# Kernel tuning notes

Measured on AMD Instinct MI355X. Metric: run time of the kernel, lower is better.

## Reference

```python
import jax, jax.numpy as jnp
import numpy as np

B = 1000        # graphs in batch
T_PER = 250     # tasks per graph
M_PER = 50      # machines per graph
N_T = B * T_PER
N_M = B * M_PER
D_T = 16        # INPUT_TASK_DIM
D_M = 8         # INPUT_MACHINE_DIM
H = 128         # hidden_dim
IN_PREV_IDX = 0
TASK_FEAT_IDX = 1
EPS = 1e-5      # BatchNorm eps


def _mk_params(rng):
    def lin(i, o):
        return (rng.standard_normal((i, o)).astype(np.float32) / np.sqrt(i),
                np.zeros(o, np.float32))
    p = {}
    p['bn_t_gamma'] = np.ones(D_T, np.float32); p['bn_t_beta'] = np.zeros(D_T, np.float32)
    p['Wt1'], p['bt1'] = lin(D_T, H); p['Wt2'], p['bt2'] = lin(H, H)
    p['bn_m_gamma'] = np.ones(D_M, np.float32); p['bn_m_beta'] = np.zeros(D_M, np.float32)
    p['Wm1'], p['bm1'] = lin(D_M, H); p['Wm2'], p['bm2'] = lin(H, H)
    p['Wa1'], p['ba1'] = lin(2 * H, H); p['Wa2'], p['ba2'] = lin(H, H)
    p['Wl1'], p['bl1'] = lin(3 * H, H); p['Wl2'], p['bl2'] = lin(H, H)
    p['Wo1'], p['bo1'] = lin(H, H); p['Wo2'], p['bo2'] = lin(H, 1)
    return p


def setup_inputs() -> dict:
    rng = np.random.default_rng(0)
    xt = rng.standard_normal((N_T, D_T)).astype(np.float32)
    # prev-task flag: even task ids are 'prev'
    xt[:, IN_PREV_IDX] = (np.arange(N_T) % 2 == 0).astype(np.float32)
    # per-graph machine assignment in [0, M_PER), or -1 (unassigned) every 10th task
    lm = rng.integers(0, M_PER, N_T)
    lm[np.arange(N_T) % 10 == 0] = -1
    xt[:, TASK_FEAT_IDX] = lm.astype(np.float32)
    xm = rng.standard_normal((N_M, D_M)).astype(np.float32)
    inp = {'x_tasks': jnp.asarray(xt), 'x_machines': jnp.asarray(xm)}
    inp.update({k: jnp.asarray(v) for k, v in _mk_params(rng).items()})
    inp['x_tasks_batch'] = jnp.asarray(np.repeat(np.arange(B), T_PER).astype(np.int32))
    inp['x_machines_batch'] = jnp.asarray(np.repeat(np.arange(B), M_PER).astype(np.int32))
    # labels are tasks 0,5,10,...; prev tasks are even ids -> prev-local index t//2
    # label tasks that are prev: t % 10 == 0 -> prev_tasks_label_idx = 5*arange(N_T//10)
    inp['label_idx'] = jnp.asarray((5 * np.arange(N_T // 10)).astype(np.int32))
    inp['num_graphs'] = B
    return inp


def _bn(x, g, b):
    # BatchNorm1d in training mode: biased batch stats
    mu = x.mean(axis=0)
    var = x.var(axis=0)
    return g * (x - mu) * jax.lax.rsqrt(var + EPS) + b


def _seg_mean(x, seg, n):
    s = jax.ops.segment_sum(x, seg, num_segments=n)
    c = jax.ops.segment_sum(jnp.ones((x.shape[0], 1), x.dtype), seg, num_segments=n)
    return s / jnp.maximum(c, 1.0)


def reference(x_tasks, x_machines, bn_t_gamma, bn_t_beta, Wt1, bt1, Wt2, bt2,
              bn_m_gamma, bn_m_beta, Wm1, bm1, Wm2, bm2,
              Wa1, ba1, Wa2, ba2, Wl1, bl1, Wl2, bl2,
              Wo1, bo1, Wo2, bo2,
              x_tasks_batch, x_machines_batch, label_idx, num_graphs):
    nm = x_machines.shape[0]
    # tasks_select_assignment: local machine id -> global machine row (or pad row nm)
    tm_col = x_tasks[:, TASK_FEAT_IDX]
    cnt_m = jnp.bincount(x_machines_batch, length=num_graphs)
    cum = jnp.cumsum(cnt_m) - cnt_m  # cumulative machines per graph
    task_m = jnp.where(tm_col == -1.0, nm,
                       tm_col.astype(jnp.int32) + cum[x_tasks_batch].astype(jnp.int32))
    # node embeddings: BN -> Linear -> ReLU -> Linear -> ReLU
    th = jax.nn.relu(jax.nn.relu(_bn(x_tasks, bn_t_gamma, bn_t_beta) @ Wt1 + bt1) @ Wt2 + bt2)
    mh = jax.nn.relu(jax.nn.relu(_bn(x_machines, bn_m_gamma, bn_m_beta) @ Wm1 + bm1) @ Wm2 + bm2)
    # global aggregation per graph (scatter_mean) + MLP
    aggr = jnp.concatenate([_seg_mean(th, x_tasks_batch, num_graphs),
                            _seg_mean(mh, x_machines_batch, num_graphs)], axis=1)
    aggr = jax.nn.relu(aggr @ Wa1 + ba1) @ Wa2 + ba2
    # gather machine embedding per task (pad row of zeros for unassigned)
    mh_pad = jnp.concatenate([mh, jnp.zeros((1, H), mh.dtype)], axis=0)
    cat = jnp.concatenate([th, aggr[x_tasks_batch], mh_pad[task_m]], axis=1)  # [N_T, 3H]
    h = jax.nn.relu(cat @ Wl1 + bl1) @ Wl2 + bl2
    out = (jax.nn.relu(h @ Wo1 + bo1) @ Wo2 + bo2)[label_idx]
    return out
```

## Files before the change

### kernel.cpp

```cpp
#include <hip/hip_runtime.h>
#include <hip/hip_bf16.h>

constexpr int B     = 1000;
constexpr int T_PER = 250;
constexpr int M_PER = 50;
constexpr int N_T   = B * T_PER;
constexpr int N_M   = B * M_PER;
constexpr int H     = 128;
constexpr int N_LBL = 25000;
constexpr float EPS = 1e-05f;

constexpr int NB_T = 256;
constexpr int NB_M = 64;
constexpr int NB_P = 64;

constexpr int OFF_PART_T = 0;
constexpr int OFF_PART_M = OFF_PART_T + NB_T * 32;
constexpr int OFF_AT     = OFF_PART_M + NB_M * 16;
constexpr int OFF_BT     = OFF_AT + 16;
constexpr int OFF_AM     = OFF_BT + 16;
constexpr int OFF_BM     = OFF_AM + 8;
constexpr int OFF_BT1F   = OFF_BM + 8;
constexpr int OFF_BM1F   = OFF_BT1F + 128;
constexpr int OFF_MEANT  = OFF_BM1F + 128;
constexpr int OFF_MEANM  = OFF_MEANT + B * H;
constexpr int OFF_HALF   = OFF_MEANM + B * H;
constexpr int HO_WT1  = 0;
constexpr int HO_WT2  = 4096;
constexpr int HO_WM1  = 20480;
constexpr int HO_WM2  = 24576;
constexpr int HO_WA1  = 40960;
constexpr int HO_WA2  = 73728;
constexpr int HO_WL1  = 90112;
constexpr int HO_WL2  = 139264;
constexpr int HO_WO1  = 155648;

typedef _Float16 f16x8 __attribute__((ext_vector_type(8)));
typedef _Float16 f16x4 __attribute__((ext_vector_type(4)));
typedef float f32x4 __attribute__((ext_vector_type(4)));

#define MFMA16(a, b, c) __builtin_amdgcn_mfma_f32_16x16x32_f16(a, b, c, 0, 0, 0)

template <int C, int NB>
__device__ __forceinline__ void stats_body(const float* __restrict__ x, int nelem,
                                           float* __restrict__ part, int blk, int t,
                                           float* ls, float* lq) {
    float s = 0.f, q = 0.f;
    for (int e = blk * 256 + t; e < nelem; e += NB * 256) {
        float v = x[e];
        s += v;
        q += v * v;
    }
    ls[t] = s; lq[t] = q;
    __syncthreads();
    if (t < C) {
        float S = 0.f, Q = 0.f;
        for (int u = t; u < 256; u += C) { S += ls[u]; Q += lq[u]; }
        part[blk * 2 * C + t] = S;
        part[blk * 2 * C + C + t] = Q;
    }
}

__device__ __forceinline__ void cvt_tr(const float* __restrict__ src, _Float16* __restrict__ dst,
                                       int K, int Kp, int tid, int nt) {
    for (int idx = tid; idx < 128 * Kp; idx += nt) {
        int c = idx / Kp, k = idx - c * Kp;
        float v = (k < K) ? src[k * 128 + c] : 0.f;
        dst[idx] = (_Float16)v;
    }
}

__global__ __launch_bounds__(256) void stats_prep_kernel(
        const float* __restrict__ xt, const float* __restrict__ xm,
        const float* __restrict__ Wt1, const float* __restrict__ Wt2,
        const float* __restrict__ Wm1, const float* __restrict__ Wm2,
        const float* __restrict__ Wa1, const float* __restrict__ Wa2,
        const float* __restrict__ Wl1, const float* __restrict__ Wl2,
        const float* __restrict__ Wo1,
        float* __restrict__ wsf, _Float16* __restrict__ wh) {
    __shared__ float ls[256], lq[256];
    const int bid = blockIdx.x, t = threadIdx.x;
    if (bid < NB_T) {
        stats_body<16, NB_T>(xt, N_T * 16, wsf + OFF_PART_T, bid, t, ls, lq);
    } else if (bid < NB_T + NB_M) {
        stats_body<8, NB_M>(xm, N_M * 8, wsf + OFF_PART_M, bid - NB_T, t, ls, lq);
    } else {
        const int tid = (bid - NB_T - NB_M) * 256 + t;
        const int nt = NB_P * 256;
        cvt_tr(Wt1, wh + HO_WT1, 16, 32, tid, nt);
        cvt_tr(Wt2, wh + HO_WT2, 128, 128, tid, nt);
        cvt_tr(Wm1, wh + HO_WM1, 8, 32, tid, nt);
        cvt_tr(Wm2, wh + HO_WM2, 128, 128, tid, nt);
        cvt_tr(Wa1, wh + HO_WA1, 256, 256, tid, nt);
        cvt_tr(Wa2, wh + HO_WA2, 128, 128, tid, nt);
        cvt_tr(Wl1, wh + HO_WL1, 384, 384, tid, nt);
        cvt_tr(Wl2, wh + HO_WL2, 128, 128, tid, nt);
        cvt_tr(Wo1, wh + HO_WO1, 128, 128, tid, nt);
    }
}

__global__ __launch_bounds__(256) void finalize_kernel(
        const float* __restrict__ gt, const float* __restrict__ btb,
        const float* __restrict__ gm, const float* __restrict__ bmb,
        const float* __restrict__ Wt1, const float* __restrict__ bt1,
        const float* __restrict__ Wm1, const float* __restrict__ bm1,
        float* __restrict__ ws) {
    __shared__ float red[256];
    __shared__ float statT[32], statM[16];
    __shared__ float shT[16], shM[8];
    const int t = threadIdx.x;
    {
        const int slot = t & 31, chunk = t >> 5;
        const float* p = ws + OFF_PART_T;
        float s = 0.f;
        for (int b = chunk * 32; b < chunk * 32 + 32; b++) s += p[b * 32 + slot];
        red[t] = s;
    }
    __syncthreads();
    if (t < 32) {
        float v = 0.f;
#pragma unroll
        for (int c = 0; c < 8; c++) v += red[t + 32 * c];
        statT[t] = v;
    }
    __syncthreads();
    {
        float s = 0.f;
        if (t < 128) {
            const int slot = t & 15, chunk = t >> 4;
            const float* p = ws + OFF_PART_M;
            for (int b = chunk * 8; b < chunk * 8 + 8; b++) s += p[b * 16 + slot];
        }
        red[t] = s;
    }
    __syncthreads();
    if (t < 16) {
        float v = 0.f;
#pragma unroll
        for (int c = 0; c < 8; c++) v += red[t + 16 * c];
        statM[t] = v;
    }
    __syncthreads();
    if (t < 16) {
        float mu  = statT[t] / (float)N_T;
        float var = statT[16 + t] / (float)N_T - mu * mu;
        float a   = gt[t] * rsqrtf(var + EPS);
        ws[OFF_AT + t] = a;
        float b = btb[t] - mu * a;
        ws[OFF_BT + t] = b;
        shT[t] = b;
    } else if (t < 24) {
        int c = t - 16;
        float mu  = statM[c] / (float)N_M;
        float var = statM[8 + c] / (float)N_M - mu * mu;
        float a   = gm[c] * rsqrtf(var + EPS);
        ws[OFF_AM + c] = a;
        float b = bmb[c] - mu * a;
        ws[OFF_BM + c] = b;
        shM[c] = b;
    }
    __syncthreads();
    if (t < 128) {
        float s = bt1[t];
#pragma unroll
        for (int k = 0; k < 16; k++) s += shT[k] * Wt1[k * 128 + t];
        ws[OFF_BT1F + t] = s;
    } else {
        int c = t - 128;
        float s = bm1[c];
#pragma unroll
        for (int k = 0; k < 8; k++) s += shM[k] * Wm1[k * 128 + c];
        ws[OFF_BM1F + c] = s;
    }
}

__device__ __forceinline__ void zacc(f32x4 acc[4][2]) {
#pragma unroll
    for (int rg = 0; rg < 4; rg++)
#pragma unroll
        for (int mi = 0; mi < 2; mi++) acc[rg][mi] = (f32x4){0.f, 0.f, 0.f, 0.f};
}

__device__ __forceinline__ void ld32(f16x8 w[2], const _Float16* __restrict__ WT,
                                     int m0, int r, int gq) {
#pragma unroll
    for (int mi = 0; mi < 2; mi++)
        w[mi] = *(const f16x8*)(WT + ((m0 + mi) * 16 + r) * 32 + gq * 8);
}

__device__ __forceinline__ void ld128(f16x8 w[2][4], const _Float16* __restrict__ WT,
                                      int lda, int k0, int m0, int r, int gq) {
#pragma unroll
    for (int mi = 0; mi < 2; mi++)
#pragma unroll
        for (int ks = 0; ks < 4; ks++)
            w[mi][ks] = *(const f16x8*)(WT + ((m0 + mi) * 16 + r) * lda + k0 + ks * 32 + gq * 8);
}

__device__ __forceinline__ void mm32(const f16x8 w[2], const _Float16* __restrict__ act,
                                     int rstride, int r, int gq, f32x4 acc[4][2]) {
#pragma unroll
    for (int rg = 0; rg < 4; rg++) {
        const f16x8 bf = *(const f16x8*)(act + (rg * 16 + r) * rstride + gq * 8);
        acc[rg][0] = MFMA16(w[0], bf, acc[rg][0]);
        acc[rg][1] = MFMA16(w[1], bf, acc[rg][1]);
    }
}

__device__ __forceinline__ void mm128(const f16x8 w[2][4], const _Float16* __restrict__ act,
                                      int rstride, int r, int gq, f32x4 acc[4][2]) {
#pragma unroll
    for (int rg = 0; rg < 4; rg++)
#pragma unroll
        for (int ks = 0; ks < 4; ks++) {
            const f16x8 bf = *(const f16x8*)(act + (rg * 16 + r) * rstride + ks * 32 + gq * 8);
            acc[rg][0] = MFMA16(w[0][ks], bf, acc[rg][0]);
            acc[rg][1] = MFMA16(w[1][ks], bf, acc[rg][1]);
        }
}

__device__ __forceinline__ void epi_cs(const f32x4 acc[4][2], const f32x4 bv[2],
                                       _Float16* __restrict__ dst, int dstride,
                                       int m0, int r, int gq, bool relu) {
#pragma unroll
    for (int rg = 0; rg < 4; rg++)
#pragma unroll
        for (int mi = 0; mi < 2; mi++) {
            f16x4 hv;
#pragma unroll
            for (int j = 0; j < 4; j++) {
                float v = acc[rg][mi][j] + bv[mi][j];
                if (relu) v = fmaxf(v, 0.f);
                hv[j] = (_Float16)v;
            }
            *(f16x4*)(dst + (rg * 16 + r) * dstride + (m0 + mi) * 16 + gq * 4) = hv;
        }
}

template <int CIN, int ROWS, int PASSES>
__device__ __forceinline__ void seg_body(const float* __restrict__ x, const float* __restrict__ scaleA,
        const _Float16* __restrict__ W1T, const float* __restrict__ b1,
        const _Float16* __restrict__ W2T, const float* __restrict__ b2,
        float* __restrict__ meanout, int g, int t,
        _Float16* __restrict__ xs, _Float16* __restrict__ h1s) {
    const int lane = t & 63, wave = t >> 6;
    const int r = lane & 15, gq = lane >> 4;
    const int m0 = 2 * wave;
    f16x8 w1[2], w2[2][4];
    ld32(w1, W1T, m0, r, gq);
    ld128(w2, W2T, 128, 0, m0, r, gq);
    f32x4 b1v[2], b2v[2];
#pragma unroll
    for (int mi = 0; mi < 2; mi++) {
        b1v[mi] = *(const f32x4*)(b1 + (m0 + mi) * 16 + gq * 4);
        b2v[mi] = *(const f32x4*)(b2 + (m0 + mi) * 16 + gq * 4);
    }
    const int jrow = (CIN == 16) ? (t >> 2) : (t >> 1);
    const int part = (CIN == 16) ? (t & 3) : (t & 1);
    const bool stager = (CIN == 16) ? true : (t < 128);
    f32x4 av = {0.f, 0.f, 0.f, 0.f};
    if (stager) av = *(const f32x4*)(scaleA + part * 4);
    f16x4 z4; z4[0] = z4[1] = z4[2] = z4[3] = (_Float16)0.f;
    if (stager) {
        if (CIN == 16) {
            *(f16x4*)(xs + jrow * 40 + 16 + part * 4) = z4;
        } else {
#pragma unroll
            for (int q = 0; q < 3; q++)
                *(f16x4*)(xs + jrow * 40 + 8 + part * 12 + q * 4) = z4;
        }
    }
    float4 xr = {0.f, 0.f, 0.f, 0.f};
    if (stager) {
        int cl = (jrow < ROWS) ? jrow : (ROWS - 1);
        xr = *(const float4*)(x + (g * ROWS + cl) * CIN + part * 4);
    }
    f32x4 rs[2];
    rs[0] = (f32x4){0.f, 0.f, 0.f, 0.f};
    rs[1] = (f32x4){0.f, 0.f, 0.f, 0.f};
    for (int p = 0; p < PASSES; p++) {
        if (stager) {
            const bool valid = (p * 64 + jrow) < ROWS;
            f16x4 hv;
            hv[0] = (_Float16)(valid ? av[0] * xr.x : 0.f);
            hv[1] = (_Float16)(valid ? av[1] * xr.y : 0.f);
            hv[2] = (_Float16)(valid ? av[2] * xr.z : 0.f);
            hv[3] = (_Float16)(valid ? av[3] * xr.w : 0.f);
            *(f16x4*)(xs + jrow * 40 + part * 4) = hv;
        }
        __syncthreads();
        if (p + 1 < PASSES && stager) {
            int lr = (p + 1) * 64 + jrow;
            int cl = (lr < ROWS) ? lr : (ROWS - 1);
            xr = *(const float4*)(x + (g * ROWS + cl) * CIN + part * 4);
        }
        f32x4 acc[4][2];
        zacc(acc);
        mm32(w1, xs, 40, r, gq, acc);
        epi_cs(acc, b1v, h1s, 136, m0, r, gq, true);
        __syncthreads();
        zacc(acc);
        mm128(w2, h1s, 136, r, gq, acc);
#pragma unroll
        for (int rg = 0; rg < 4; rg++) {
            const bool vr = (p * 64 + rg * 16 + r) < ROWS;
#pragma unroll
            for (int mi = 0; mi < 2; mi++)
#pragma unroll
                for (int j = 0; j < 4; j++) {
                    float v = fmaxf(acc[rg][mi][j] + b2v[mi][j], 0.f);
                    rs[mi][j] += vr ? v : 0.f;
                }
        }
    }
#pragma unroll
    for (int mi = 0; mi < 2; mi++)
#pragma unroll
        for (int j = 0; j < 4; j++) {
            float v = rs[mi][j];
            v += __shfl_xor(v, 1); v += __shfl_xor(v, 2);
            v += __shfl_xor(v, 4); v += __shfl_xor(v, 8);
            rs[mi][j] = v;
        }
    if (r == 0) {
        constexpr float inv = 1.f / (float)ROWS;
#pragma unroll
        for (int mi = 0; mi < 2; mi++) {
            f32x4 st = rs[mi] * inv;
            *(f32x4*)(meanout + g * H + (m0 + mi) * 16 + gq * 4) = st;
        }
    }
}

__global__ __launch_bounds__(256) void seg_fused(const float* __restrict__ xt, const float* __restrict__ xm,
        const _Float16* __restrict__ wh, const float* __restrict__ wsf,
        const float* __restrict__ bt2, const float* __restrict__ bm2,
        float* __restrict__ meanT, float* __restrict__ meanM) {
    __shared__ __attribute__((aligned(16))) _Float16 xs[64 * 40];
    __shared__ __attribute__((aligned(16))) _Float16 h1s[64 * 136];
    if (blockIdx.x < B)
        seg_body<16, T_PER, 4>(xt, wsf + OFF_AT, wh + HO_WT1, wsf + OFF_BT1F,
                               wh + HO_WT2, bt2, meanT, blockIdx.x, threadIdx.x, xs, h1s);
    else
        seg_body<8, M_PER, 1>(xm, wsf + OFF_AM, wh + HO_WM1, wsf + OFF_BM1F,
                              wh + HO_WM2, bm2, meanM, blockIdx.x - B, threadIdx.x, xs, h1s);
}

__global__ __launch_bounds__(256) void aggr_kernel(const float* __restrict__ meanT, const float* __restrict__ meanM,
        const _Float16* __restrict__ Wa1T, const float* __restrict__ ba1,
        const _Float16* __restrict__ Wa2T, const float* __restrict__ ba2,
        const _Float16* __restrict__ Wl1T, const float* __restrict__ bl1,
        float* __restrict__ agg2) {
    __shared__ __attribute__((aligned(16))) _Float16 cin[16 * 264];
    __shared__ __attribute__((aligned(16))) _Float16 h1s[16 * 136];
    __shared__ __attribute__((aligned(16))) _Float16 ags[16 * 136];
    const int t = threadIdx.x, lane = t & 63, wave = t >> 6;
    const int r = lane & 15, gq = lane >> 4;
    const int m0 = 2 * wave;
    const int g0 = blockIdx.x * 16;
    f16x8 wa1[2][8], wa2[2][4], wl1b[2][4];
#pragma unroll
    for (int mi = 0; mi < 2; mi++)
#pragma unroll
        for (int ks = 0; ks < 8; ks++)
            wa1[mi][ks] = *(const f16x8*)(Wa1T + ((m0 + mi) * 16 + r) * 256 + ks * 32 + gq * 8);
    ld128(wa2, Wa2T, 128, 0, m0, r, gq);
    ld128(wl1b, Wl1T, 384, 128, m0, r, gq);
    f32x4 b1v[2], b2v[2], blv[2];
#pragma unroll
    for (int mi = 0; mi < 2; mi++) {
        b1v[mi] = *(const f32x4*)(ba1 + (m0 + mi) * 16 + gq * 4);
        b2v[mi] = *(const f32x4*)(ba2 + (m0 + mi) * 16 + gq * 4);
        blv[mi] = *(const f32x4*)(bl1 + (m0 + mi) * 16 + gq * 4);
    }
    for (int e = t; e < 16 * 64; e += 256) {
        int j = e >> 6, c4 = e & 63;
        int g = g0 + j;
        float4 v = {0.f, 0.f, 0.f, 0.f};
        if (g < B) v = (c4 < 32) ? *(const float4*)(meanT + g * H + c4 * 4)
                                 : *(const float4*)(meanM + g * H + (c4 - 32) * 4);
        f16x4 hv;
        hv[0] = (_Float16)v.x; hv[1] = (_Float16)v.y; hv[2] = (_Float16)v.z; hv[3] = (_Float16)v.w;
        *(f16x4*)(cin + j * 264 + c4 * 4) = hv;
    }
    __syncthreads();
    f32x4 a0 = {0.f, 0.f, 0.f, 0.f}, a1 = {0.f, 0.f, 0.f, 0.f};
    {
        const _Float16* bp = cin + r * 264 + gq * 8;
#pragma unroll
        for (int ks = 0; ks < 8; ks++) {
            const f16x8 bf = *(const f16x8*)(bp + ks * 32);
            a0 = MFMA16(wa1[0][ks], bf, a0);
            a1 = MFMA16(wa1[1][ks], bf, a1);
        }
    }
    {
        f16x4 h0, h1v;
#pragma unroll
        for (int j = 0; j < 4; j++) {
            h0[j]  = (_Float16)fmaxf(a0[j] + b1v[0][j], 0.f);
            h1v[j] = (_Float16)fmaxf(a1[j] + b1v[1][j], 0.f);
        }
        *(f16x4*)(h1s + r * 136 + m0 * 16 + gq * 4) = h0;
        *(f16x4*)(h1s + r * 136 + (m0 + 1) * 16 + gq * 4) = h1v;
    }
    __syncthreads();
    a0 = (f32x4){0.f, 0.f, 0.f, 0.f}; a1 = (f32x4){0.f, 0.f, 0.f, 0.f};
    {
        const _Float16* bp = h1s + r * 136 + gq * 8;
#pragma unroll
        for (int ks = 0; ks < 4; ks++) {
            const f16x8 bf = *(const f16x8*)(bp + ks * 32);
            a0 = MFMA16(wa2[0][ks], bf, a0);
            a1 = MFMA16(wa2[1][ks], bf, a1);
        }
    }
    {
        f16x4 h0, h1v;
#pragma unroll
        for (int j = 0; j < 4; j++) {
            h0[j]  = (_Float16)(a0[j] + b2v[0][j]);
            h1v[j] = (_Float16)(a1[j] + b2v[1][j]);
        }
        *(f16x4*)(ags + r * 136 + m0 * 16 + gq * 4) = h0;
        *(f16x4*)(ags + r * 136 + (m0 + 1) * 16 + gq * 4) = h1v;
    }
    __syncthreads();
    a0 = (f32x4){0.f, 0.f, 0.f, 0.f}; a1 = (f32x4){0.f, 0.f, 0.f, 0.f};
    {
        const _Float16* bp = ags + r * 136 + gq * 8;
#pragma unroll
        for (int ks = 0; ks < 4; ks++) {
            const f16x8 bf = *(const f16x8*)(bp + ks * 32);
            a0 = MFMA16(wl1b[0][ks], bf, a0);
            a1 = MFMA16(wl1b[1][ks], bf, a1);
        }
    }
    if (g0 + r < B) {
        *(f32x4*)(agg2 + (g0 + r) * H + m0 * 16 + gq * 4) = a0 + blv[0];
        *(f32x4*)(agg2 + (g0 + r) * H + (m0 + 1) * 16 + gq * 4) = a1 + blv[1];
    }
}

__global__ __launch_bounds__(256) void label_kernel(
        const float* __restrict__ xt, const float* __restrict__ xm,
        const float* __restrict__ scT, const float* __restrict__ scM,
        const _Float16* __restrict__ Wt1T, const float* __restrict__ bt1f,
        const _Float16* __restrict__ Wt2T, const float* __restrict__ bt2,
        const _Float16* __restrict__ Wm1T, const float* __restrict__ bm1f,
        const _Float16* __restrict__ Wm2T, const float* __restrict__ bm2,
        const _Float16* __restrict__ Wl1T,
        const _Float16* __restrict__ Wl2T, const float* __restrict__ bl2,
        const _Float16* __restrict__ Wo1T, const float* __restrict__ bo1,
        const float* __restrict__ Wo2, const float* __restrict__ bo2,
        const float* __restrict__ agg2,
        const int* __restrict__ tbatch, const int* __restrict__ lidx,
        float* __restrict__ out) {
    __shared__ __attribute__((aligned(16))) _Float16 xs_t[64 * 40];
    __shared__ __attribute__((aligned(16))) _Float16 xs_m[64 * 40];
    __shared__ __attribute__((aligned(16))) _Float16 h1s[64 * 136];
    __shared__ __attribute__((aligned(16))) _Float16 cat[64 * 264];
    __shared__ float psum[4][64];
    __shared__ int ridx[64], gidx[64], midx[64];
    const int t = threadIdx.x;
    const int lane = t & 63, wave = t >> 6;
    const int r = lane & 15, gq = lane >> 4;
    const int m0 = 2 * wave;
    if (t < 64) {
        int i = blockIdx.x * 64 + t;
        int rr = (i < N_LBL) ? lidx[i] : 0;
        ridx[t] = rr;
        int gg = tbatch[rr];
        gidx[t] = gg;
        float tv = xt[rr * 16 + 1];
        midx[t] = (tv == -1.0f) ? -1 : ((int)tv + gg * M_PER);
    }
    __syncthreads();
    f16x4 z4; z4[0] = z4[1] = z4[2] = z4[3] = (_Float16)0.f;
    {
        int j = t >> 2, part = t & 3;
        f32x4 avt = *(const f32x4*)(scT + part * 4);
        float4 v = *(const float4*)(xt + ridx[j] * 16 + part * 4);
        f16x4 hv;
        hv[0] = (_Float16)(avt[0] * v.x); hv[1] = (_Float16)(avt[1] * v.y);
        hv[2] = (_Float16)(avt[2] * v.z); hv[3] = (_Float16)(avt[3] * v.w);
        *(f16x4*)(xs_t + j * 40 + part * 4) = hv;
        *(f16x4*)(xs_t + j * 40 + 16 + part * 4) = z4;
    }
    if (t < 128) {
        int j = t >> 1, part = t & 1;
        f32x4 avm = *(const f32x4*)(scM + part * 4);
        int m = midx[j];
        f16x4 hv = z4;
        if (m >= 0) {
            float4 v = *(const float4*)(xm + m * 8 + part * 4);
            hv[0] = (_Float16)(avm[0] * v.x); hv[1] = (_Float16)(avm[1] * v.y);
            hv[2] = (_Float16)(avm[2] * v.z); hv[3] = (_Float16)(avm[3] * v.w);
        }
        *(f16x4*)(xs_m + j * 40 + part * 4) = hv;
#pragma unroll
        for (int q = 0; q < 3; q++)
            *(f16x4*)(xs_m + j * 40 + 8 + part * 12 + q * 4) = z4;
    }
    __syncthreads();
    f32x4 agg2v[4][2];
#pragma unroll
    for (int rg = 0; rg < 4; rg++)
#pragma unroll
        for (int mi = 0; mi < 2; mi++)
            agg2v[rg][mi] = *(const f32x4*)(agg2 + gidx[rg * 16 + r] * H + (m0 + mi) * 16 + gq * 4);
    f32x4 acc[4][2];
    f16x8 wt1[2]; ld32(wt1, Wt1T, m0, r, gq);
    f16x8 wt2[2][4]; ld128(wt2, Wt2T, 128, 0, m0, r, gq);
    f32x4 bva[2], bvb[2];
#pragma unroll
    for (int mi = 0; mi < 2; mi++) {
        bva[mi] = *(const f32x4*)(bt1f + (m0 + mi) * 16 + gq * 4);
        bvb[mi] = *(const f32x4*)(bt2 + (m0 + mi) * 16 + gq * 4);
    }
    zacc(acc);
    mm32(wt1, xs_t, 40, r, gq, acc);
    epi_cs(acc, bva, h1s, 136, m0, r, gq, true);
    f16x8 wm1[2]; ld32(wm1, Wm1T, m0, r, gq);
    __syncthreads();
    zacc(acc);
    mm128(wt2, h1s, 136, r, gq, acc);
    epi_cs(acc, bvb, cat, 264, m0, r, gq, true);
    f16x8 wm2[2][4]; ld128(wm2, Wm2T, 128, 0, m0, r, gq);
    __syncthreads();
#pragma unroll
    for (int mi = 0; mi < 2; mi++) {
        bva[mi] = *(const f32x4*)(bm1f + (m0 + mi) * 16 + gq * 4);
        bvb[mi] = *(const f32x4*)(bm2 + (m0 + mi) * 16 + gq * 4);
    }
    zacc(acc);
    mm32(wm1, xs_m, 40, r, gq, acc);
    epi_cs(acc, bva, h1s, 136, m0, r, gq, true);
    f16x8 wl1a[2][4]; ld128(wl1a, Wl1T, 384, 0, m0, r, gq);
    __syncthreads();
    zacc(acc);
    mm128(wm2, h1s, 136, r, gq, acc);
#pragma unroll
    for (int rg = 0; rg < 4; rg++) {
        const bool sent = (midx[rg * 16 + r] < 0);
#pragma unroll
        for (int mi = 0; mi < 2; mi++) {
            f16x4 hv;
#pragma unroll
            for (int j = 0; j < 4; j++) {
                float v = fmaxf(acc[rg][mi][j] + bvb[mi][j], 0.f);
                hv[j] = (_Float16)(sent ? 0.f : v);
            }
            *(f16x4*)(cat + (rg * 16 + r) * 264 + 128 + (m0 + mi) * 16 + gq * 4) = hv;
        }
    }
    f16x8 wl1c[2][4]; ld128(wl1c, Wl1T, 384, 256, m0, r, gq);
    __syncthreads();
    zacc(acc);
    mm128(wl1a, cat, 264, r, gq, acc);
    mm128(wl1c, cat + 128, 264, r, gq, acc);
#pragma unroll
    for (int rg = 0; rg < 4; rg++)
#pragma unroll
        for (int mi = 0; mi < 2; mi++) {
            f16x4 hv;
#pragma unroll
            for (int j = 0; j < 4; j++)
                hv[j] = (_Float16)fmaxf(acc[rg][mi][j] + agg2v[rg][mi][j], 0.f);
            *(f16x4*)(h1s + (rg * 16 + r) * 136 + (m0 + mi) * 16 + gq * 4) = hv;
        }
    f16x8 wl2[2][4]; ld128(wl2, Wl2T, 128, 0, m0, r, gq);
    __syncthreads();
#pragma unroll
    for (int mi = 0; mi < 2; mi++) bva[mi] = *(const f32x4*)(bl2 + (m0 + mi) * 16 + gq * 4);
    zacc(acc);
    mm128(wl2, h1s, 136, r, gq, acc);
    epi_cs(acc, bva, cat, 264, m0, r, gq, false);
    f16x8 wo1[2][4]; ld128(wo1, Wo1T, 128, 0, m0, r, gq);
    __syncthreads();
#pragma unroll
    for (int mi = 0; mi < 2; mi++) bva[mi] = *(const f32x4*)(bo1 + (m0 + mi) * 16 + gq * 4);
    f32x4 wo2v[2];
#pragma unroll
    for (int mi = 0; mi < 2; mi++) wo2v[mi] = *(const f32x4*)(Wo2 + (m0 + mi) * 16 + gq * 4);
    zacc(acc);
    mm128(wo1, cat, 264, r, gq, acc);
#pragma unroll
    for (int rg = 0; rg < 4; rg++) {
        float pv = 0.f;
#pragma unroll
        for (int mi = 0; mi < 2; mi++)
#pragma unroll
            for (int j = 0; j < 4; j++)
                pv += fmaxf(acc[rg][mi][j] + bva[mi][j], 0.f) * wo2v[mi][j];
        pv += __shfl_xor(pv, 16);
        pv += __shfl_xor(pv, 32);
        if (lane < 16) psum[wave][rg * 16 + lane] = pv;
    }
    __syncthreads();
    if (t < 64) {
        int i = blockIdx.x * 64 + t;
        if (i < N_LBL)
            out[i] = psum[0][t] + psum[1][t] + psum[2][t] + psum[3][t] + bo2[0];
    }
}

extern "C" void kernel_launch(void* const* d_in, const int* in_sizes, int n_in,
                              void* d_out, int out_size, void* d_ws, size_t ws_size,
                              hipStream_t stream) {
    const float* xt  = (const float*)d_in[0];
    const float* xm  = (const float*)d_in[1];
    const float* gt  = (const float*)d_in[2];
    const float* btb = (const float*)d_in[3];
    const float* Wt1 = (const float*)d_in[4];  const float* bt1 = (const float*)d_in[5];
    const float* Wt2 = (const float*)d_in[6];  const float* bt2 = (const float*)d_in[7];
    const float* gm  = (const float*)d_in[8];  const float* bmb = (const float*)d_in[9];
    const float* Wm1 = (const float*)d_in[10]; const float* bm1 = (const float*)d_in[11];
    const float* Wm2 = (const float*)d_in[12]; const float* bm2 = (const float*)d_in[13];
    const float* Wa1 = (const float*)d_in[14]; const float* ba1 = (const float*)d_in[15];
    const float* Wa2 = (const float*)d_in[16]; const float* ba2 = (const float*)d_in[17];
    const float* Wl1 = (const float*)d_in[18]; const float* bl1 = (const float*)d_in[19];
    const float* Wl2 = (const float*)d_in[20]; const float* bl2 = (const float*)d_in[21];
    const float* Wo1 = (const float*)d_in[22]; const float* bo1 = (const float*)d_in[23];
    const float* Wo2 = (const float*)d_in[24]; const float* bo2 = (const float*)d_in[25];
    const int* tb  = (const int*)d_in[26];
    const int* lix = (const int*)d_in[28];
    float* wsf = (float*)d_ws;
    _Float16* wh = (_Float16*)(wsf + OFF_HALF);
    float* outp = (float*)d_out;

    stats_prep_kernel<<<NB_T + NB_M + NB_P, 256, 0, stream>>>(
        xt, xm, Wt1, Wt2, Wm1, Wm2, Wa1, Wa2, Wl1, Wl2, Wo1, wsf, wh);
    finalize_kernel<<<1, 256, 0, stream>>>(gt, btb, gm, bmb, Wt1, bt1, Wm1, bm1, wsf);
    seg_fused<<<2 * B, 256, 0, stream>>>(xt, xm, wh, wsf, bt2, bm2,
                                         wsf + OFF_MEANT, wsf + OFF_MEANM);
    aggr_kernel<<<(B + 15) / 16, 256, 0, stream>>>(wsf + OFF_MEANT, wsf + OFF_MEANM,
                                                   wh + HO_WA1, ba1, wh + HO_WA2, ba2,
                                                   wh + HO_WL1, bl1, wsf + OFF_MEANT);
    label_kernel<<<(N_LBL + 63) / 64, 256, 0, stream>>>(xt, xm,
                                                        wsf + OFF_AT, wsf + OFF_AM,
                                                        wh + HO_WT1, wsf + OFF_BT1F, wh + HO_WT2, bt2,
                                                        wh + HO_WM1, wsf + OFF_BM1F, wh + HO_WM2, bm2,
                                                        wh + HO_WL1,
                                                        wh + HO_WL2, bl2,
                                                        wh + HO_WO1, bo1, Wo2, bo2,
                                                        wsf + OFF_MEANT, tb, lix, outp);
}
```

Baseline: 74.12 us.

## Rewrite segment-mean MLP as per-wave register-resident MFMA pipeline with pre-converted fp16 inputs

```diff
diff --git a/kernel.cpp b/kernel.cpp
--- a/kernel.cpp
+++ b/kernel.cpp
@@ -1,5 +1,4 @@
 #include <hip/hip_runtime.h>
-#include <hip/hip_bf16.h>
 
 constexpr int B     = 1000;
 constexpr int T_PER = 250;
@@ -34,15 +33,19 @@
 constexpr int HO_WL1  = 90112;
 constexpr int HO_WL2  = 139264;
 constexpr int HO_WO1  = 155648;
+constexpr int HO_XT16 = 172032;
+constexpr int HO_XM16 = HO_XT16 + N_T * 16;
 
 typedef _Float16 f16x8 __attribute__((ext_vector_type(8)));
 typedef _Float16 f16x4 __attribute__((ext_vector_type(4)));
 typedef float f32x4 __attribute__((ext_vector_type(4)));
 
-#define MFMA16(a, b, c) __builtin_amdgcn_mfma_f32_16x16x32_f16(a, b, c, 0, 0, 0)
+#define MFMA16(a, b, c)   __builtin_amdgcn_mfma_f32_16x16x32_f16(a, b, c, 0, 0, 0)
+#define MFMAK16(a, b, c)  __builtin_amdgcn_mfma_f32_16x16x16f16(a, b, c, 0, 0, 0)
 
 template <int C, int NB>
-__device__ __forceinline__ void stats_body(const float* __restrict__ x, int nelem,
+__device__ __forceinline__ void stats_body(const float* __restrict__ x,
+                                           _Float16* __restrict__ x16, int nelem,
                                            float* __restrict__ part, int blk, int t,
                                            float* ls, float* lq) {
     float s = 0.f, q = 0.f;
@@ -50,6 +53,7 @@
         float v = x[e];
         s += v;
         q += v * v;
+        x16[e] = (_Float16)v;
     }
     ls[t] = s; lq[t] = q;
     __syncthreads();
@@ -72,8 +76,8 @@
 
 __global__ __launch_bounds__(256) void stats_prep_kernel(
         const float* __restrict__ xt, const float* __restrict__ xm,
-        const float* __restrict__ Wt1, const float* __restrict__ Wt2,
-        const float* __restrict__ Wm1, const float* __restrict__ Wm2,
+        _Float16* __restrict__ xt16, _Float16* __restrict__ xm16,
+        const float* __restrict__ Wt2, const float* __restrict__ Wm2,
         const float* __restrict__ Wa1, const float* __restrict__ Wa2,
         const float* __restrict__ Wl1, const float* __restrict__ Wl2,
         const float* __restrict__ Wo1,
@@ -81,15 +85,13 @@
     __shared__ float ls[256], lq[256];
     const int bid = blockIdx.x, t = threadIdx.x;
     if (bid < NB_T) {
-        stats_body<16, NB_T>(xt, N_T * 16, wsf + OFF_PART_T, bid, t, ls, lq);
+        stats_body<16, NB_T>(xt, xt16, N_T * 16, wsf + OFF_PART_T, bid, t, ls, lq);
     } else if (bid < NB_T + NB_M) {
-        stats_body<8, NB_M>(xm, N_M * 8, wsf + OFF_PART_M, bid - NB_T, t, ls, lq);
+        stats_body<8, NB_M>(xm, xm16, N_M * 8, wsf + OFF_PART_M, bid - NB_T, t, ls, lq);
     } else {
         const int tid = (bid - NB_T - NB_M) * 256 + t;
         const int nt = NB_P * 256;
-        cvt_tr(Wt1, wh + HO_WT1, 16, 32, tid, nt);
         cvt_tr(Wt2, wh + HO_WT2, 128, 128, tid, nt);
-        cvt_tr(Wm1, wh + HO_WM1, 8, 32, tid, nt);
         cvt_tr(Wm2, wh + HO_WM2, 128, 128, tid, nt);
         cvt_tr(Wa1, wh + HO_WA1, 256, 256, tid, nt);
         cvt_tr(Wa2, wh + HO_WA2, 128, 128, tid, nt);
@@ -104,10 +106,11 @@
         const float* __restrict__ gm, const float* __restrict__ bmb,
         const float* __restrict__ Wt1, const float* __restrict__ bt1,
         const float* __restrict__ Wm1, const float* __restrict__ bm1,
-        float* __restrict__ ws) {
+        float* __restrict__ ws, _Float16* __restrict__ wh) {
     __shared__ float red[256];
     __shared__ float statT[32], statM[16];
     __shared__ float shT[16], shM[8];
+    __shared__ float saT[16], saM[8];
     const int t = threadIdx.x;
     {
         const int slot = t & 31, chunk = t >> 5;
@@ -149,6 +152,7 @@
         float b = btb[t] - mu * a;
         ws[OFF_BT + t] = b;
         shT[t] = b;
+        saT[t] = a;
     } else if (t < 24) {
         int c = t - 16;
         float mu  = statM[c] / (float)N_M;
@@ -158,6 +162,7 @@
         float b = bmb[c] - mu * a;
         ws[OFF_BM + c] = b;
         shM[c] = b;
+        saM[c] = a;
     }
     __syncthreads();
     if (t < 128) {
@@ -165,12 +170,34 @@
 #pragma unroll
         for (int k = 0; k < 16; k++) s += shT[k] * Wt1[k * 128 + t];
         ws[OFF_BT1F + t] = s;
+        _Float16 row[32];
+#pragma unroll
+        for (int k = 0; k < 16; k++) row[k] = (_Float16)(Wt1[k * 128 + t] * saT[k]);
+        float bh = (float)(_Float16)s;
+        row[16] = (_Float16)s;
+        row[17] = (_Float16)(s - bh);
+#pragma unroll
+        for (int k = 18; k < 32; k++) row[k] = (_Float16)0.f;
+#pragma unroll
+        for (int q = 0; q < 4; q++)
+            *(f16x8*)(wh + HO_WT1 + t * 32 + q * 8) = *(const f16x8*)(row + q * 8);
     } else {
         int c = t - 128;
         float s = bm1[c];
 #pragma unroll
         for (int k = 0; k < 8; k++) s += shM[k] * Wm1[k * 128 + c];
         ws[OFF_BM1F + c] = s;
+        _Float16 row[32];
+#pragma unroll
+        for (int k = 0; k < 8; k++) row[k] = (_Float16)(Wm1[k * 128 + c] * saM[k]);
+        float bh = (float)(_Float16)s;
+        row[8] = (_Float16)s;
+        row[9] = (_Float16)(s - bh);
+#pragma unroll
+        for (int k = 10; k < 32; k++) row[k] = (_Float16)0.f;
+#pragma unroll
+        for (int q = 0; q < 4; q++)
+            *(f16x8*)(wh + HO_WM1 + c * 32 + q * 8) = *(const f16x8*)(row + q * 8);
     }
 }
 
@@ -237,84 +264,77 @@
         }
 }
 
-template <int CIN, int ROWS, int PASSES>
-__device__ __forceinline__ void seg_body(const float* __restrict__ x, const float* __restrict__ scaleA,
-        const _Float16* __restrict__ W1T, const float* __restrict__ b1,
-        const _Float16* __restrict__ W2T, const float* __restrict__ b2,
-        float* __restrict__ meanout, int g, int t,
-        _Float16* __restrict__ xs, _Float16* __restrict__ h1s) {
-    const int lane = t & 63, wave = t >> 6;
+__global__ __launch_bounds__(256, 2) void seg_wave(
+        const _Float16* __restrict__ xt16, const _Float16* __restrict__ xm16,
+        const _Float16* __restrict__ wh,
+        const float* __restrict__ bt2, const float* __restrict__ bm2,
+        float* __restrict__ meanT, float* __restrict__ meanM) {
+    const int t = threadIdx.x, lane = t & 63, w = t >> 6;
     const int r = lane & 15, gq = lane >> 4;
-    const int m0 = 2 * wave;
-    f16x8 w1[2], w2[2][4];
-    ld32(w1, W1T, m0, r, gq);
-    ld128(w2, W2T, 128, 0, m0, r, gq);
-    f32x4 b1v[2], b2v[2];
-#pragma unroll
-    for (int mi = 0; mi < 2; mi++) {
-        b1v[mi] = *(const f32x4*)(b1 + (m0 + mi) * 16 + gq * 4);
-        b2v[mi] = *(const f32x4*)(b2 + (m0 + mi) * 16 + gq * 4);
-    }
-    const int jrow = (CIN == 16) ? (t >> 2) : (t >> 1);
-    const int part = (CIN == 16) ? (t & 3) : (t & 1);
-    const bool stager = (CIN == 16) ? true : (t < 128);
-    f32x4 av = {0.f, 0.f, 0.f, 0.f};
-    if (stager) av = *(const f32x4*)(scaleA + part * 4);
-    f16x4 z4; z4[0] = z4[1] = z4[2] = z4[3] = (_Float16)0.f;
-    if (stager) {
-        if (CIN == 16) {
-            *(f16x4*)(xs + jrow * 40 + 16 + part * 4) = z4;
-        } else {
-#pragma unroll
-            for (int q = 0; q < 3; q++)
-                *(f16x4*)(xs + jrow * 40 + 8 + part * 12 + q * 4) = z4;
-        }
-    }
-    float4 xr = {0.f, 0.f, 0.f, 0.f};
-    if (stager) {
-        int cl = (jrow < ROWS) ? jrow : (ROWS - 1);
-        xr = *(const float4*)(x + (g * ROWS + cl) * CIN + part * 4);
-    }
-    f32x4 rs[2];
-    rs[0] = (f32x4){0.f, 0.f, 0.f, 0.f};
-    rs[1] = (f32x4){0.f, 0.f, 0.f, 0.f};
-    for (int p = 0; p < PASSES; p++) {
-        if (stager) {
-            const bool valid = (p * 64 + jrow) < ROWS;
-            f16x4 hv;
-            hv[0] = (_Float16)(valid ? av[0] * xr.x : 0.f);
-            hv[1] = (_Float16)(valid ? av[1] * xr.y : 0.f);
-            hv[2] = (_Float16)(valid ? av[2] * xr.z : 0.f);
-            hv[3] = (_Float16)(valid ? av[3] * xr.w : 0.f);
-            *(f16x4*)(xs + jrow * 40 + part * 4) = hv;
-        }
-        __syncthreads();
-        if (p + 1 < PASSES && stager) {
-            int lr = (p + 1) * 64 + jrow;
-            int cl = (lr < ROWS) ? lr : (ROWS - 1);
-            xr = *(const float4*)(x + (g * ROWS + cl) * CIN + part * 4);
-        }
-        f32x4 acc[4][2];
-        zacc(acc);
-        mm32(w1, xs, 40, r, gq, acc);
-        epi_cs(acc, b1v, h1s, 136, m0, r, gq, true);
-        __syncthreads();
-        zacc(acc);
-        mm128(w2, h1s, 136, r, gq, acc);
-#pragma unroll
-        for (int rg = 0; rg < 4; rg++) {
-            const bool vr = (p * 64 + rg * 16 + r) < ROWS;
-#pragma unroll
-            for (int mi = 0; mi < 2; mi++)
-#pragma unroll
-                for (int j = 0; j < 4; j++) {
-                    float v = fmaxf(acc[rg][mi][j] + b2v[mi][j], 0.f);
-                    rs[mi][j] += vr ? v : 0.f;
-                }
-        }
-    }
-#pragma unroll
-    for (int mi = 0; mi < 2; mi++)
+    const bool taskw = (((w >> 1) ^ (blockIdx.x & 1)) == 0);
+    const int g = blockIdx.x * 2 + (w & 1);
+    const _Float16* W1T = wh + (taskw ? HO_WT1 : HO_WM1);
+    const _Float16* W2T = wh + (taskw ? HO_WT2 : HO_WM2);
+    const float* b2 = taskw ? bt2 : bm2;
+    const _Float16* x16 = taskw ? xt16 : xm16;
+    float* mout = taskw ? meanT : meanM;
+    const int ROWS = taskw ? T_PER : M_PER;
+    const int CIN  = taskw ? 16 : 8;
+    const int NIT  = taskw ? 16 : 4;
+    f16x8 w1[8];
+#pragma unroll
+    for (int mi = 0; mi < 8; mi++)
+        w1[mi] = *(const f16x8*)(W1T + (mi * 16 + r) * 32 + gq * 8);
+    f16x4 w2[8][8];
+#pragma unroll
+    for (int mi = 0; mi < 8; mi++)
+#pragma unroll
+        for (int ks = 0; ks < 8; ks++)
+            w2[mi][ks] = *(const f16x4*)(W2T + (mi * 16 + r) * 128 + ks * 16 + gq * 4);
+    f16x8 xconst;
+#pragma unroll
+    for (int e = 0; e < 8; e++) xconst[e] = (_Float16)0.f;
+    const int biasgq = taskw ? 2 : 1;
+    if (gq == biasgq) { xconst[0] = (_Float16)1.f; xconst[1] = (_Float16)1.f; }
+    const bool loader = (gq * 8 < CIN);
+    const f32x4 zf = (f32x4){0.f, 0.f, 0.f, 0.f};
+    f32x4 rs[8];
+#pragma unroll
+    for (int mi = 0; mi < 8; mi++) rs[mi] = zf;
+    for (int it = 0; it < NIT; it++) {
+        const int row = it * 16 + r;
+        const int cl = (row < ROWS) ? row : (ROWS - 1);
+        f16x8 xb = xconst;
+        if (loader) xb = *(const f16x8*)(x16 + (g * ROWS + cl) * CIN + gq * 8);
+        f16x4 bb[8];
+#pragma unroll
+        for (int mi = 0; mi < 8; mi++) {
+            f32x4 a1 = MFMA16(w1[mi], xb, zf);
+            f16x4 h;
+#pragma unroll
+            for (int j = 0; j < 4; j++) h[j] = (_Float16)fmaxf(a1[j], 0.f);
+            bb[mi] = h;
+        }
+        const bool full = (it + 1) * 16 <= ROWS;
+#pragma unroll
+        for (int mi = 0; mi < 8; mi++) {
+            f32x4 a2 = zf;
+#pragma unroll
+            for (int ks = 0; ks < 8; ks++) a2 = MFMAK16(w2[mi][ks], bb[ks], a2);
+            const f32x4 bv = *(const f32x4*)(b2 + mi * 16 + gq * 4);
+            if (full) {
+#pragma unroll
+                for (int j = 0; j < 4; j++) rs[mi][j] += fmaxf(a2[j] + bv[j], 0.f);
+            } else {
+                const float mk = (row < ROWS) ? 1.f : 0.f;
+#pragma unroll
+                for (int j = 0; j < 4; j++)
+                    rs[mi][j] = fmaf(fmaxf(a2[j] + bv[j], 0.f), mk, rs[mi][j]);
+            }
+        }
+    }
+#pragma unroll
+    for (int mi = 0; mi < 8; mi++)
 #pragma unroll
         for (int j = 0; j < 4; j++) {
             float v = rs[mi][j];
@@ -323,27 +343,13 @@
             rs[mi][j] = v;
         }
     if (r == 0) {
-        constexpr float inv = 1.f / (float)ROWS;
-#pragma unroll
-        for (int mi = 0; mi < 2; mi++) {
+        const float inv = 1.f / (float)ROWS;
+#pragma unroll
+        for (int mi = 0; mi < 8; mi++) {
             f32x4 st = rs[mi] * inv;
-            *(f32x4*)(meanout + g * H + (m0 + mi) * 16 + gq * 4) = st;
-        }
-    }
-}
-
-__global__ __launch_bounds__(256) void seg_fused(const float* __restrict__ xt, const float* __restrict__ xm,
-        const _Float16* __restrict__ wh, const float* __restrict__ wsf,
-        const float* __restrict__ bt2, const float* __restrict__ bm2,
-        float* __restrict__ meanT, float* __restrict__ meanM) {
-    __shared__ __attribute__((aligned(16))) _Float16 xs[64 * 40];
-    __shared__ __attribute__((aligned(16))) _Float16 h1s[64 * 136];
-    if (blockIdx.x < B)
-        seg_body<16, T_PER, 4>(xt, wsf + OFF_AT, wh + HO_WT1, wsf + OFF_BT1F,
-                               wh + HO_WT2, bt2, meanT, blockIdx.x, threadIdx.x, xs, h1s);
-    else
-        seg_body<8, M_PER, 1>(xm, wsf + OFF_AM, wh + HO_WM1, wsf + OFF_BM1F,
-                              wh + HO_WM2, bm2, meanM, blockIdx.x - B, threadIdx.x, xs, h1s);
+            *(f32x4*)(mout + g * H + mi * 16 + gq * 4) = st;
+        }
+    }
 }
 
 __global__ __launch_bounds__(256) void aggr_kernel(const float* __restrict__ meanT, const float* __restrict__ meanM,
@@ -443,8 +449,8 @@
 }
 
 __global__ __launch_bounds__(256) void label_kernel(
-        const float* __restrict__ xt, const float* __restrict__ xm,
-        const float* __restrict__ scT, const float* __restrict__ scM,
+        const float* __restrict__ xt,
+        const _Float16* __restrict__ xt16, const _Float16* __restrict__ xm16,
         const _Float16* __restrict__ Wt1T, const float* __restrict__ bt1f,
         const _Float16* __restrict__ Wt2T, const float* __restrict__ bt2,
         const _Float16* __restrict__ Wm1T, const float* __restrict__ bm1f,
@@ -479,24 +485,15 @@
     f16x4 z4; z4[0] = z4[1] = z4[2] = z4[3] = (_Float16)0.f;
     {
         int j = t >> 2, part = t & 3;
-        f32x4 avt = *(const f32x4*)(scT + part * 4);
-        float4 v = *(const float4*)(xt + ridx[j] * 16 + part * 4);
-        f16x4 hv;
-        hv[0] = (_Float16)(avt[0] * v.x); hv[1] = (_Float16)(avt[1] * v.y);
-        hv[2] = (_Float16)(avt[2] * v.z); hv[3] = (_Float16)(avt[3] * v.w);
+        f16x4 hv = *(const f16x4*)(xt16 + ridx[j] * 16 + part * 4);
         *(f16x4*)(xs_t + j * 40 + part * 4) = hv;
         *(f16x4*)(xs_t + j * 40 + 16 + part * 4) = z4;
     }
     if (t < 128) {
         int j = t >> 1, part = t & 1;
-        f32x4 avm = *(const f32x4*)(scM + part * 4);
         int m = midx[j];
         f16x4 hv = z4;
-        if (m >= 0) {
-            float4 v = *(const float4*)(xm + m * 8 + part * 4);
-            hv[0] = (_Float16)(avm[0] * v.x); hv[1] = (_Float16)(avm[1] * v.y);
-            hv[2] = (_Float16)(avm[2] * v.z); hv[3] = (_Float16)(avm[3] * v.w);
-        }
+        if (m >= 0) hv = *(const f16x4*)(xm16 + m * 8 + part * 4);
         *(f16x4*)(xs_m + j * 40 + part * 4) = hv;
 #pragma unroll
         for (int q = 0; q < 3; q++)
@@ -627,18 +624,19 @@
     const int* lix = (const int*)d_in[28];
     float* wsf = (float*)d_ws;
     _Float16* wh = (_Float16*)(wsf + OFF_HALF);
+    _Float16* xt16 = wh + HO_XT16;
+    _Float16* xm16 = wh + HO_XM16;
     float* outp = (float*)d_out;
 
     stats_prep_kernel<<<NB_T + NB_M + NB_P, 256, 0, stream>>>(
-        xt, xm, Wt1, Wt2, Wm1, Wm2, Wa1, Wa2, Wl1, Wl2, Wo1, wsf, wh);
-    finalize_kernel<<<1, 256, 0, stream>>>(gt, btb, gm, bmb, Wt1, bt1, Wm1, bm1, wsf);
-    seg_fused<<<2 * B, 256, 0, stream>>>(xt, xm, wh, wsf, bt2, bm2,
-                                         wsf + OFF_MEANT, wsf + OFF_MEANM);
+        xt, xm, xt16, xm16, Wt2, Wm2, Wa1, Wa2, Wl1, Wl2, Wo1, wsf, wh);
+    finalize_kernel<<<1, 256, 0, stream>>>(gt, btb, gm, bmb, Wt1, bt1, Wm1, bm1, wsf, wh);
+    seg_wave<<<B / 2, 256, 0, stream>>>(xt16, xm16, wh, bt2, bm2,
+                                        wsf + OFF_MEANT, wsf + OFF_MEANM);
     aggr_kernel<<<(B + 15) / 16, 256, 0, stream>>>(wsf + OFF_MEANT, wsf + OFF_MEANM,
                                                    wh + HO_WA1, ba1, wh + HO_WA2, ba2,
                                                    wh + HO_WL1, bl1, wsf + OFF_MEANT);
-    label_kernel<<<(N_LBL + 63) / 64, 256, 0, stream>>>(xt, xm,
-                                                        wsf + OFF_AT, wsf + OFF_AM,
+    label_kernel<<<(N_LBL + 63) / 64, 256, 0, stream>>>(xt, xt16, xm16,
                                                         wh + HO_WT1, wsf + OFF_BT1F, wh + HO_WT2, bt2,
                                                         wh + HO_WM1, wsf + OFF_BM1F, wh + HO_WM2, bm2,
                                                         wh + HO_WL1,
```

Result: slower. 114.7 us (+54.7%).
